# Performance work log

Measured on AMD Instinct MI355X. Metric: run time of the kernel, lower is better.

## Reference

```python
import jax, jax.numpy as jnp
import numpy as np

B, S, D = 2, 2048, 2048
N_HEADS = 16
HEAD_DIM = D // N_HEADS  # 128


def apply_rotary(xq, xk, cos, sin):
    # xq, xk: [B, S, H, HD]; cos, sin: [S, HD//2]
    def rot(t):
        tr = t.reshape(t.shape[:-1] + (HEAD_DIM // 2, 2))
        r, i = tr[..., 0], tr[..., 1]
        c = cos[None, :, None, :]  # [1, S, 1, HD//2]
        s = sin[None, :, None, :]
        out_r = r * c - i * s
        out_i = r * s + i * c
        return jnp.stack([out_r, out_i], axis=-1).reshape(t.shape)
    return rot(xq), rot(xk)


def setup_inputs() -> dict:
    key = jax.random.key(0)
    k1, k2, k3 = jax.random.split(key, 3)
    x = jax.random.normal(k1, (B, S, D), dtype=jnp.float32)
    wqkv = jax.random.normal(k2, (3 * D, D), dtype=jnp.float32) * (D ** -0.5)
    wo = jax.random.normal(k3, (D, D), dtype=jnp.float32) * (D ** -0.5)
    # rotary tables, standard llama theta=10000
    inv_freq = 1.0 / (10000.0 ** (jnp.arange(0, HEAD_DIM, 2, dtype=jnp.float32) / HEAD_DIM))
    t = jnp.arange(S, dtype=jnp.float32)
    freqs = jnp.outer(t, inv_freq)  # [S, HD//2]
    freqs_cos = jnp.cos(freqs)
    freqs_sin = jnp.sin(freqs)
    # causal additive mask [1, 1, S, S]
    causal = jnp.tril(jnp.ones((S, S), dtype=bool))
    mask = jnp.where(causal, 0.0, -jnp.inf).astype(jnp.float32)[None, None]
    return {"x": x, "freqs_cos": freqs_cos, "freqs_sin": freqs_sin,
            "mask": mask, "wqkv": wqkv, "wo": wo, "input_pos": 0}


def reference(x, freqs_cos, freqs_sin, mask, wqkv, wo, input_pos):
    # fused QKV projection (Linear: x @ W^T)
    qkv = jnp.einsum('bsd,ed->bse', x, wqkv)  # [B, S, 3D]
    xq, xk, xv = jnp.split(qkv, 3, axis=-1)
    xq = xq.reshape(B, S, N_HEADS, HEAD_DIM)
    xk = xk.reshape(B, S, N_HEADS, HEAD_DIM)
    xv = xv.reshape(B, S, N_HEADS, HEAD_DIM)
    xq, xk = apply_rotary(xq, xk, freqs_cos, freqs_sin)
    # SDPA (kv_cache is None; input_pos unused)
    scale = HEAD_DIM ** -0.5
    scores = jnp.einsum('bqhd,bkhd->bhqk', xq, xk) * scale + mask
    attn = jax.nn.softmax(scores, axis=-1)
    out = jnp.einsum('bhqk,bkhd->bqhd', attn, xv).reshape(B, S, D)
    return jnp.einsum('bsd,ed->bse', out, wo)
```

## Files before the change

kernel.cpp:

```cpp
#include <hip/hip_runtime.h>

#define B_ 2
#define S_ 2048
#define D_ 2048
#define H_ 16
#define DH_ 128
#define E3_ (3*D_)

typedef __attribute__((ext_vector_type(4))) float f32x4;
typedef __attribute__((ext_vector_type(8))) short bf16x8;

__device__ __forceinline__ unsigned short f2bf(float f) {
  unsigned u = __float_as_uint(f);
  u += 0x7fff + ((u >> 16) & 1);
  return (unsigned short)(u >> 16);
}
__device__ __forceinline__ float bf2f(unsigned short h) {
  return __uint_as_float(((unsigned)h) << 16);
}
__device__ __forceinline__ unsigned cvt_pk_bf16(float lo, float hi) {
  unsigned r;
  asm("v_cvt_pk_bf16_f32 %0, %1, %2" : "=v"(r) : "v"(lo), "v"(hi));
  return r;
}

__global__ void cast_f32_bf16(const float* __restrict__ in, unsigned short* __restrict__ out, int n4) {
  int i = blockIdx.x * 256 + threadIdx.x;
  if (i >= n4) return;
  float4 v = reinterpret_cast<const float4*>(in)[i];
  ushort4 o;
  o.x = f2bf(v.x); o.y = f2bf(v.y); o.z = f2bf(v.z); o.w = f2bf(v.w);
  reinterpret_cast<ushort4*>(out)[i] = o;
}

template<typename OutT>
__global__ __launch_bounds__(256) void gemm_bt(const unsigned short* __restrict__ A,
                                               const unsigned short* __restrict__ Bm,
                                               OutT* __restrict__ C,
                                               unsigned short* __restrict__ Vt,
                                               int Mdim, int Ndim, int Kdim) {
  __shared__ __align__(16) unsigned short As[128*64];
  __shared__ __align__(16) unsigned short Bs[128*64];
  const int t = threadIdx.x;
  const int lane = t & 63;
  const int w = t >> 6;
  const int wm = w >> 1, wn = w & 1;
  const int l16 = lane & 15, lg = lane >> 4;
  const int bm = blockIdx.y, bn = blockIdx.x;

  f32x4 acc[4][4] = {};
  const int e0 = t * 8;

  for (int k0 = 0; k0 < Kdim; k0 += 64) {
#pragma unroll
    for (int it = 0; it < 4; ++it) {
      int e = e0 + it * 2048;
      int row = e >> 6;
      int g = (e >> 3) & 7;
      int gs = g ^ (row & 7);
      const unsigned short* ga = A  + (size_t)(bm*128 + row) * Kdim + k0 + gs*8;
      const unsigned short* gb = Bm + (size_t)(bn*128 + row) * Kdim + k0 + gs*8;
      __builtin_amdgcn_global_load_lds((const __attribute__((address_space(1))) unsigned int*)ga,
                                       (__attribute__((address_space(3))) unsigned int*)(&As[e]), 16, 0, 0);
      __builtin_amdgcn_global_load_lds((const __attribute__((address_space(1))) unsigned int*)gb,
                                       (__attribute__((address_space(3))) unsigned int*)(&Bs[e]), 16, 0, 0);
    }
    __syncthreads();
#pragma unroll
    for (int kk = 0; kk < 2; ++kk) {
      bf16x8 a[4], b[4];
#pragma unroll
      for (int mi = 0; mi < 4; ++mi) {
        int row = wm*64 + mi*16 + l16;
        int gw = kk*4 + lg;
        a[mi] = *reinterpret_cast<const bf16x8*>(&As[row*64 + ((gw ^ (row & 7))<<3)]);
      }
#pragma unroll
      for (int ni = 0; ni < 4; ++ni) {
        int row = wn*64 + ni*16 + l16;
        int gw = kk*4 + lg;
        b[ni] = *reinterpret_cast<const bf16x8*>(&Bs[row*64 + ((gw ^ (row & 7))<<3)]);
      }
#pragma unroll
      for (int mi = 0; mi < 4; ++mi)
#pragma unroll
        for (int ni = 0; ni < 4; ++ni)
          acc[mi][ni] = __builtin_amdgcn_mfma_f32_16x16x32_bf16(a[mi], b[ni], acc[mi][ni], 0, 0, 0);
    }
    __syncthreads();
  }
  if constexpr (sizeof(OutT) == 2) {
    if (Vt != nullptr && bn >= 32) {
#pragma unroll
      for (int mi = 0; mi < 4; ++mi) {
#pragma unroll
        for (int ni = 0; ni < 4; ++ni) {
          int colv = bn*128 + wn*64 + ni*16 + l16 - 2*D_;
          int h = colv >> 7, d = colv & 127;
          int row0 = bm*128 + wm*64 + mi*16 + lg*4;
          int b = row0 >> 11, s = row0 & 2047;
          ushort4 v4;
          v4.x = f2bf(acc[mi][ni][0]);
          v4.y = f2bf(acc[mi][ni][1]);
          v4.z = f2bf(acc[mi][ni][2]);
          v4.w = f2bf(acc[mi][ni][3]);
          *reinterpret_cast<ushort4*>(&Vt[(((size_t)(b*H_ + h))*DH_ + d)*S_ + s]) = v4;
        }
      }
      return;
    }
  }
#pragma unroll
  for (int mi = 0; mi < 4; ++mi) {
#pragma unroll
    for (int ni = 0; ni < 4; ++ni) {
      int col = bn*128 + wn*64 + ni*16 + l16;
      int row0 = bm*128 + wm*64 + mi*16 + lg*4;
#pragma unroll
      for (int r = 0; r < 4; ++r) {
        float v = acc[mi][ni][r];
        size_t idx = (size_t)(row0 + r) * Ndim + col;
        if constexpr (sizeof(OutT) == 2) C[idx] = f2bf(v);
        else C[idx] = v;
      }
    }
  }
}

__global__ void rope_qk(const unsigned short* __restrict__ qkv,
                        const float* __restrict__ cosT, const float* __restrict__ sinT,
                        unsigned short* __restrict__ Q, unsigned short* __restrict__ K) {
  const float SCL = 0.08838834764831845f * 1.4426950408889634f;
  int d = threadIdx.x;
  int h = blockIdx.x;
  int s = blockIdx.y;
  int b = blockIdx.z;
  size_t rowb = ((size_t)(b*S_ + s)) * E3_;
  int j = d >> 1;
  float c  = cosT[s*64 + j];
  float sn = sinT[s*64 + j];
  int de = d & ~1, odd = d & 1;
  float x0 = bf2f(qkv[rowb + h*DH_ + de]);
  float x1 = bf2f(qkv[rowb + h*DH_ + de + 1]);
  float oq = odd ? (x0*sn + x1*c) : (x0*c - x1*sn);
  size_t qo = (((size_t)(b*H_ + h)) * S_ + s) * DH_ + d;
  Q[qo] = f2bf(oq * SCL);
  float y0 = bf2f(qkv[rowb + D_ + h*DH_ + de]);
  float y1 = bf2f(qkv[rowb + D_ + h*DH_ + de + 1]);
  float ok = odd ? (y0*sn + y1*c) : (y0*c - y1*sn);
  K[qo] = f2bf(ok);
}

#define NQT 32
__global__ __launch_bounds__(512) void attn(const unsigned short* __restrict__ Q,
                                            const unsigned short* __restrict__ K,
                                            const unsigned short* __restrict__ Vt,
                                            unsigned short* __restrict__ O) {
  __shared__ __align__(16) unsigned short Ks[64*128];
  __shared__ __align__(16) unsigned short Vs[128*64];
  __shared__ __align__(16) unsigned short Plds[8][16*64];
  const int x = blockIdx.x;
  const int bh = blockIdx.y;
  const int b = bh >> 4, h = bh & 15;
  const int t = threadIdx.x;
  const int lane = t & 63;
  const int w = t >> 6;
  const int wg = w >> 2;
  const int wi = w & 3;
  const int l16 = lane & 15, lg = lane >> 4;
  const int qt = wg ? (NQT - 1 - x) : x;
  const int q0 = qt * 64 + wi * 16;
  const unsigned short* Qh = Q  + (size_t)bh * S_ * DH_;
  const unsigned short* Kh = K  + (size_t)bh * S_ * DH_;
  const unsigned short* Vh = Vt + (size_t)bh * DH_ * S_;

  bf16x8 aq[4];
#pragma unroll
  for (int kk = 0; kk < 4; ++kk)
    aq[kk] = *reinterpret_cast<const bf16x8*>(Qh + (size_t)(q0 + l16)*DH_ + kk*32 + lg*8);

  f32x4 o[8] = {};
  float mrun = -1e30f, lrun = 0.f;
  const int ntiles = NQT - x;

  for (int tile = 0; tile < ntiles; ++tile) {
    const int kv0 = tile * 64;
#pragma unroll
    for (int it = 0; it < 2; ++it) {
      int e = t*8 + it*4096;
      int row = e >> 7;
      int gslot = (e >> 3) & 15;
      int gsrc = gslot ^ (row & 7);
      const unsigned short* ga = Kh + (size_t)(kv0 + row) * DH_ + gsrc*8;
      __builtin_amdgcn_global_load_lds((const __attribute__((address_space(1))) unsigned int*)ga,
                                       (__attribute__((address_space(3))) unsigned int*)(&Ks[e]), 16, 0, 0);
    }
#pragma unroll
    for (int it = 0; it < 2; ++it) {
      int e = t*8 + it*4096;
      int d = e >> 6;
      int gslot = (e >> 3) & 7;
      int gsrc = gslot ^ (d & 7);
      const unsigned short* gv = Vh + (size_t)d * S_ + kv0 + gsrc*8;
      __builtin_amdgcn_global_load_lds((const __attribute__((address_space(1))) unsigned int*)gv,
                                       (__attribute__((address_space(3))) unsigned int*)(&Vs[e]), 16, 0, 0);
    }
    __syncthreads();

    if (tile <= qt) {
      f32x4 sc[4] = {};
#pragma unroll
      for (int kk = 0; kk < 4; ++kk) {
#pragma unroll
        for (int n = 0; n < 4; ++n) {
          int row = n*16 + l16;
          int g = kk*4 + lg;
          bf16x8 bk = *reinterpret_cast<const bf16x8*>(&Ks[row*128 + ((g ^ (row & 7))<<3)]);
          sc[n] = __builtin_amdgcn_mfma_f32_16x16x32_bf16(bk, aq[kk], sc[n], 0, 0, 0);
        }
      }
      if (tile == qt) {
        int qrow = q0 + l16;
#pragma unroll
        for (int n = 0; n < 4; ++n)
#pragma unroll
          for (int r = 0; r < 4; ++r) {
            int kidx = kv0 + n*16 + lg*4 + r;
            sc[n][r] = (kidx > qrow) ? -1e30f : sc[n][r];
          }
      }
      float mt = sc[0][0];
#pragma unroll
      for (int n = 0; n < 4; ++n)
#pragma unroll
        for (int r = 0; r < 4; ++r) mt = fmaxf(mt, sc[n][r]);
      mt = fmaxf(mt, __shfl_xor(mt, 16));
      mt = fmaxf(mt, __shfl_xor(mt, 32));
      if (__any(mt > mrun + 8.f)) {
        float mnew = fmaxf(mrun, mt);
        float alpha = __builtin_amdgcn_exp2f(mrun - mnew);
        mrun = mnew;
        lrun *= alpha;
        float ar[4];
#pragma unroll
        for (int r = 0; r < 4; ++r) ar[r] = __shfl(alpha, lg*4 + r);
#pragma unroll
        for (int n2 = 0; n2 < 8; ++n2)
#pragma unroll
          for (int r = 0; r < 4; ++r) o[n2][r] *= ar[r];
      }
      float rs = 0.f;
      unsigned pk[4][2];
#pragma unroll
      for (int n = 0; n < 4; ++n) {
        float p0 = __builtin_amdgcn_exp2f(sc[n][0] - mrun);
        float p1 = __builtin_amdgcn_exp2f(sc[n][1] - mrun);
        float p2 = __builtin_amdgcn_exp2f(sc[n][2] - mrun);
        float p3 = __builtin_amdgcn_exp2f(sc[n][3] - mrun);
        rs += (p0 + p1) + (p2 + p3);
        pk[n][0] = cvt_pk_bf16(p0, p1);
        pk[n][1] = cvt_pk_bf16(p2, p3);
      }
      rs += __shfl_xor(rs, 16);
      rs += __shfl_xor(rs, 32);
      lrun += rs;
      unsigned short* Pw = &Plds[w][0];
      char* Pb = (char*)Pw + l16*128;
#pragma unroll
      for (int n = 0; n < 4; ++n) {
        int sslot = (n*4 + lg) ^ (l16 & 14);
        *reinterpret_cast<uint2*>(Pb + sslot*8) = make_uint2(pk[n][0], pk[n][1]);
      }
      bf16x8 pa[2];
#pragma unroll
      for (int kk2 = 0; kk2 < 2; ++kk2) {
        int tp = (kk2*4 + lg) ^ ((l16 >> 1) & 7);
        pa[kk2] = *reinterpret_cast<const bf16x8*>(Pb + tp*16);
      }
#pragma unroll
      for (int kk2 = 0; kk2 < 2; ++kk2) {
#pragma unroll
        for (int n2 = 0; n2 < 8; ++n2) {
          int d = n2*16 + l16;
          int g = kk2*4 + lg;
          bf16x8 bv = *reinterpret_cast<const bf16x8*>(&Vs[d*64 + ((g ^ (d & 7))<<3)]);
          o[n2] = __builtin_amdgcn_mfma_f32_16x16x32_bf16(pa[kk2], bv, o[n2], 0, 0, 0);
        }
      }
    }
    __syncthreads();
  }
  float linv = 1.f / lrun;
  float lr[4];
#pragma unroll
  for (int r = 0; r < 4; ++r) lr[r] = __shfl(linv, lg*4 + r);
  size_t ob = ((size_t)b * S_) * D_;
#pragma unroll
  for (int n2 = 0; n2 < 8; ++n2) {
#pragma unroll
    for (int r = 0; r < 4; ++r) {
      int rowq = q0 + lg*4 + r;
      int d = n2*16 + l16;
      O[ob + (size_t)rowq * D_ + h*DH_ + d] = f2bf(o[n2][r] * lr[r]);
    }
  }
}

extern "C" void kernel_launch(void* const* d_in, const int* in_sizes, int n_in,
                              void* d_out, int out_size, void* d_ws, size_t ws_size,
                              hipStream_t stream) {
  const float* x    = (const float*)d_in[0];
  const float* fcos = (const float*)d_in[1];
  const float* fsin = (const float*)d_in[2];
  const float* wqkv = (const float*)d_in[4];
  const float* wo   = (const float*)d_in[5];
  float* out = (float*)d_out;
  char* ws = (char*)d_ws;

  unsigned short* xb    = (unsigned short*)(ws);
  unsigned short* wqkvb = (unsigned short*)(ws + 16777216);
  unsigned short* wob   = (unsigned short*)(ws + 41943040);
  unsigned short* qkv   = (unsigned short*)(ws + 50331648);
  unsigned short* Qb    = (unsigned short*)(ws + 100663296);
  unsigned short* Kb    = (unsigned short*)(ws + 117440512);
  unsigned short* Vtb   = (unsigned short*)(ws + 134217728);
  unsigned short* attn_out = xb;

  cast_f32_bf16<<<dim3(2097152/256), 256, 0, stream>>>(x, xb, 2097152);
  cast_f32_bf16<<<dim3(3145728/256), 256, 0, stream>>>(wqkv, wqkvb, 3145728);
  cast_f32_bf16<<<dim3(1048576/256), 256, 0, stream>>>(wo, wob, 1048576);

  gemm_bt<unsigned short><<<dim3(6144/128, 4096/128), 256, 0, stream>>>(xb, wqkvb, qkv, Vtb, 4096, 6144, 2048);
  rope_qk<<<dim3(16, 2048, 2), 128, 0, stream>>>(qkv, fcos, fsin, Qb, Kb);
  attn<<<dim3(16, 32), 512, 0, stream>>>(Qb, Kb, Vtb, attn_out);
  gemm_bt<float><<<dim3(2048/128, 4096/128), 256, 0, stream>>>(attn_out, wob, out, (unsigned short*)nullptr, 4096, 2048, 2048);
}
```

Measured before the change: 271.2 us.

## Fuse RoPE into QKV GEMM epilogue and double-buffer attention KV tiles

RoPE and the Q scaling move into the QKV GEMM epilogue, using a lane shuffle to fetch the paired element, so Q and K are written directly in head-major layout. This removes the separate rope kernel and the round trip through the intermediate qkv buffer. The attention kernel now double-buffers its K/V LDS tiles so the next tile's loads overlap compute, with one barrier per iteration. It also remaps block indices across XCDs and raises wave priority around the MFMA sections. The cost is more shared memory per block and per-element cos/sin loads in the GEMM epilogue.

```diff
diff --git a/kernel.cpp b/kernel.cpp
--- a/kernel.cpp
+++ b/kernel.cpp
@@ -33,12 +33,14 @@
   reinterpret_cast<ushort4*>(out)[i] = o;
 }
 
-template<typename OutT>
-__global__ __launch_bounds__(256) void gemm_bt(const unsigned short* __restrict__ A,
-                                               const unsigned short* __restrict__ Bm,
-                                               OutT* __restrict__ C,
-                                               unsigned short* __restrict__ Vt,
-                                               int Mdim, int Ndim, int Kdim) {
+__global__ __launch_bounds__(256) void gemm_qkv(const unsigned short* __restrict__ A,
+                                                const unsigned short* __restrict__ Bm,
+                                                unsigned short* __restrict__ Qb,
+                                                unsigned short* __restrict__ Kb,
+                                                unsigned short* __restrict__ Vt,
+                                                const float* __restrict__ cosT,
+                                                const float* __restrict__ sinT) {
+  const int Kdim = 2048;
   __shared__ __align__(16) unsigned short As[128*64];
   __shared__ __align__(16) unsigned short Bs[128*64];
   const int t = threadIdx.x;
@@ -89,26 +91,107 @@
     }
     __syncthreads();
   }
-  if constexpr (sizeof(OutT) == 2) {
-    if (Vt != nullptr && bn >= 32) {
+
+  if (bn >= 32) {
+#pragma unroll
+    for (int mi = 0; mi < 4; ++mi) {
+#pragma unroll
+      for (int ni = 0; ni < 4; ++ni) {
+        int colv = (bn - 32)*128 + wn*64 + ni*16 + l16;
+        int h = colv >> 7, d = colv & 127;
+        int row0 = bm*128 + wm*64 + mi*16 + lg*4;
+        int b = row0 >> 11, s = row0 & 2047;
+        ushort4 v4;
+        v4.x = f2bf(acc[mi][ni][0]);
+        v4.y = f2bf(acc[mi][ni][1]);
+        v4.z = f2bf(acc[mi][ni][2]);
+        v4.w = f2bf(acc[mi][ni][3]);
+        *reinterpret_cast<ushort4*>(&Vt[(((size_t)(b*H_ + h))*DH_ + d)*S_ + s]) = v4;
+      }
+    }
+  } else {
+    const float SCLQ = 0.08838834764831845f * 1.4426950408889634f;
+    const bool isQ = (bn < 16);
+    unsigned short* dst = isQ ? Qb : Kb;
+    const float sgn = (l16 & 1) ? 1.f : -1.f;
+#pragma unroll
+    for (int ni = 0; ni < 4; ++ni) {
+      int colh = (bn & 15)*128 + wn*64 + ni*16 + l16;
+      int h = colh >> 7, d = colh & 127;
+      int j = d >> 1;
 #pragma unroll
       for (int mi = 0; mi < 4; ++mi) {
-#pragma unroll
-        for (int ni = 0; ni < 4; ++ni) {
-          int colv = bn*128 + wn*64 + ni*16 + l16 - 2*D_;
-          int h = colv >> 7, d = colv & 127;
-          int row0 = bm*128 + wm*64 + mi*16 + lg*4;
-          int b = row0 >> 11, s = row0 & 2047;
-          ushort4 v4;
-          v4.x = f2bf(acc[mi][ni][0]);
-          v4.y = f2bf(acc[mi][ni][1]);
-          v4.z = f2bf(acc[mi][ni][2]);
-          v4.w = f2bf(acc[mi][ni][3]);
-          *reinterpret_cast<ushort4*>(&Vt[(((size_t)(b*H_ + h))*DH_ + d)*S_ + s]) = v4;
+        int row0 = bm*128 + wm*64 + mi*16 + lg*4;
+#pragma unroll
+        for (int r = 0; r < 4; ++r) {
+          int row = row0 + r;
+          int b = row >> 11, s = row & 2047;
+          float c  = cosT[s*64 + j];
+          float sn = sinT[s*64 + j];
+          float v = acc[mi][ni][r];
+          float p = __shfl_xor(v, 1);
+          float ov = fmaf(v, c, p * sn * sgn);
+          if (isQ) ov *= SCLQ;
+          dst[(((size_t)(b*H_ + h))*S_ + s)*DH_ + d] = f2bf(ov);
         }
       }
-      return;
-    }
+    }
+  }
+}
+
+__global__ __launch_bounds__(256) void gemm_bt(const unsigned short* __restrict__ A,
+                                               const unsigned short* __restrict__ Bm,
+                                               float* __restrict__ C,
+                                               int Ndim, int Kdim) {
+  __shared__ __align__(16) unsigned short As[128*64];
+  __shared__ __align__(16) unsigned short Bs[128*64];
+  const int t = threadIdx.x;
+  const int lane = t & 63;
+  const int w = t >> 6;
+  const int wm = w >> 1, wn = w & 1;
+  const int l16 = lane & 15, lg = lane >> 4;
+  const int bm = blockIdx.y, bn = blockIdx.x;
+
+  f32x4 acc[4][4] = {};
+  const int e0 = t * 8;
+
+  for (int k0 = 0; k0 < Kdim; k0 += 64) {
+#pragma unroll
+    for (int it = 0; it < 4; ++it) {
+      int e = e0 + it * 2048;
+      int row = e >> 6;
+      int g = (e >> 3) & 7;
+      int gs = g ^ (row & 7);
+      const unsigned short* ga = A  + (size_t)(bm*128 + row) * Kdim + k0 + gs*8;
+      const unsigned short* gb = Bm + (size_t)(bn*128 + row) * Kdim + k0 + gs*8;
+      __builtin_amdgcn_global_load_lds((const __attribute__((address_space(1))) unsigned int*)ga,
+                                       (__attribute__((address_space(3))) unsigned int*)(&As[e]), 16, 0, 0);
+      __builtin_amdgcn_global_load_lds((const __attribute__((address_space(1))) unsigned int*)gb,
+                                       (__attribute__((address_space(3))) unsigned int*)(&Bs[e]), 16, 0, 0);
+    }
+    __syncthreads();
+#pragma unroll
+    for (int kk = 0; kk < 2; ++kk) {
+      bf16x8 a[4], b[4];
+#pragma unroll
+      for (int mi = 0; mi < 4; ++mi) {
+        int row = wm*64 + mi*16 + l16;
+        int gw = kk*4 + lg;
+        a[mi] = *reinterpret_cast<const bf16x8*>(&As[row*64 + ((gw ^ (row & 7))<<3)]);
+      }
+#pragma unroll
+      for (int ni = 0; ni < 4; ++ni) {
+        int row = wn*64 + ni*16 + l16;
+        int gw = kk*4 + lg;
+        b[ni] = *reinterpret_cast<const bf16x8*>(&Bs[row*64 + ((gw ^ (row & 7))<<3)]);
+      }
+#pragma unroll
+      for (int mi = 0; mi < 4; ++mi)
+#pragma unroll
+        for (int ni = 0; ni < 4; ++ni)
+          acc[mi][ni] = __builtin_amdgcn_mfma_f32_16x16x32_bf16(a[mi], b[ni], acc[mi][ni], 0, 0, 0);
+    }
+    __syncthreads();
   }
 #pragma unroll
   for (int mi = 0; mi < 4; ++mi) {
@@ -117,38 +200,10 @@
       int col = bn*128 + wn*64 + ni*16 + l16;
       int row0 = bm*128 + wm*64 + mi*16 + lg*4;
 #pragma unroll
-      for (int r = 0; r < 4; ++r) {
-        float v = acc[mi][ni][r];
-        size_t idx = (size_t)(row0 + r) * Ndim + col;
-        if constexpr (sizeof(OutT) == 2) C[idx] = f2bf(v);
-        else C[idx] = v;
-      }
-    }
-  }
-}
-
-__global__ void rope_qk(const unsigned short* __restrict__ qkv,
-                        const float* __restrict__ cosT, const float* __restrict__ sinT,
-                        unsigned short* __restrict__ Q, unsigned short* __restrict__ K) {
-  const float SCL = 0.08838834764831845f * 1.4426950408889634f;
-  int d = threadIdx.x;
-  int h = blockIdx.x;
-  int s = blockIdx.y;
-  int b = blockIdx.z;
-  size_t rowb = ((size_t)(b*S_ + s)) * E3_;
-  int j = d >> 1;
-  float c  = cosT[s*64 + j];
-  float sn = sinT[s*64 + j];
-  int de = d & ~1, odd = d & 1;
-  float x0 = bf2f(qkv[rowb + h*DH_ + de]);
-  float x1 = bf2f(qkv[rowb + h*DH_ + de + 1]);
-  float oq = odd ? (x0*sn + x1*c) : (x0*c - x1*sn);
-  size_t qo = (((size_t)(b*H_ + h)) * S_ + s) * DH_ + d;
-  Q[qo] = f2bf(oq * SCL);
-  float y0 = bf2f(qkv[rowb + D_ + h*DH_ + de]);
-  float y1 = bf2f(qkv[rowb + D_ + h*DH_ + de + 1]);
-  float ok = odd ? (y0*sn + y1*c) : (y0*c - y1*sn);
-  K[qo] = f2bf(ok);
+      for (int r = 0; r < 4; ++r)
+        C[(size_t)(row0 + r) * Ndim + col] = acc[mi][ni][r];
+    }
+  }
 }
 
 #define NQT 32
@@ -156,19 +211,21 @@
                                             const unsigned short* __restrict__ K,
                                             const unsigned short* __restrict__ Vt,
                                             unsigned short* __restrict__ O) {
-  __shared__ __align__(16) unsigned short Ks[64*128];
-  __shared__ __align__(16) unsigned short Vs[128*64];
+  __shared__ __align__(16) unsigned short Ks[2][64*128];
+  __shared__ __align__(16) unsigned short Vs[2][128*64];
   __shared__ __align__(16) unsigned short Plds[8][16*64];
-  const int x = blockIdx.x;
-  const int bh = blockIdx.y;
+  const int orig = blockIdx.y * gridDim.x + blockIdx.x;
+  const int wg = (orig & 7) * 64 + (orig >> 3);
+  const int x = wg & 15;
+  const int bh = wg >> 4;
   const int b = bh >> 4, h = bh & 15;
   const int t = threadIdx.x;
   const int lane = t & 63;
   const int w = t >> 6;
-  const int wg = w >> 2;
+  const int wg8 = w >> 2;
   const int wi = w & 3;
   const int l16 = lane & 15, lg = lane >> 4;
-  const int qt = wg ? (NQT - 1 - x) : x;
+  const int qt = wg8 ? (NQT - 1 - x) : x;
   const int q0 = qt * 64 + wi * 16;
   const unsigned short* Qh = Q  + (size_t)bh * S_ * DH_;
   const unsigned short* Kh = K  + (size_t)bh * S_ * DH_;
@@ -183,42 +240,55 @@
   float mrun = -1e30f, lrun = 0.f;
   const int ntiles = NQT - x;
 
+#define STAGE_KV(TILE)                                                                              \
+  {                                                                                                 \
+    const int kv0s = (TILE) * 64;                                                                   \
+    unsigned short* Kd = &Ks[(TILE) & 1][0];                                                        \
+    unsigned short* Vd = &Vs[(TILE) & 1][0];                                                        \
+    _Pragma("unroll")                                                                               \
+    for (int it = 0; it < 2; ++it) {                                                                \
+      int e = t*8 + it*4096;                                                                        \
+      int row = e >> 7;                                                                             \
+      int gslot = (e >> 3) & 15;                                                                    \
+      int gsrc = gslot ^ (row & 7);                                                                 \
+      const unsigned short* ga = Kh + (size_t)(kv0s + row) * DH_ + gsrc*8;                          \
+      __builtin_amdgcn_global_load_lds((const __attribute__((address_space(1))) unsigned int*)ga,   \
+                                       (__attribute__((address_space(3))) unsigned int*)(&Kd[e]), 16, 0, 0); \
+    }                                                                                               \
+    _Pragma("unroll")                                                                               \
+    for (int it = 0; it < 2; ++it) {                                                                \
+      int e = t*8 + it*4096;                                                                        \
+      int dd = e >> 6;                                                                              \
+      int gslot = (e >> 3) & 7;                                                                     \
+      int gsrc = gslot ^ (dd & 7);                                                                  \
+      const unsigned short* gv = Vh + (size_t)dd * S_ + kv0s + gsrc*8;                              \
+      __builtin_amdgcn_global_load_lds((const __attribute__((address_space(1))) unsigned int*)gv,   \
+                                       (__attribute__((address_space(3))) unsigned int*)(&Vd[e]), 16, 0, 0); \
+    }                                                                                               \
+  }
+
+  STAGE_KV(0);
+
   for (int tile = 0; tile < ntiles; ++tile) {
+    __syncthreads();
+    if (tile + 1 < ntiles) STAGE_KV(tile + 1);
     const int kv0 = tile * 64;
-#pragma unroll
-    for (int it = 0; it < 2; ++it) {
-      int e = t*8 + it*4096;
-      int row = e >> 7;
-      int gslot = (e >> 3) & 15;
-      int gsrc = gslot ^ (row & 7);
-      const unsigned short* ga = Kh + (size_t)(kv0 + row) * DH_ + gsrc*8;
-      __builtin_amdgcn_global_load_lds((const __attribute__((address_space(1))) unsigned int*)ga,
-                                       (__attribute__((address_space(3))) unsigned int*)(&Ks[e]), 16, 0, 0);
-    }
-#pragma unroll
-    for (int it = 0; it < 2; ++it) {
-      int e = t*8 + it*4096;
-      int d = e >> 6;
-      int gslot = (e >> 3) & 7;
-      int gsrc = gslot ^ (d & 7);
-      const unsigned short* gv = Vh + (size_t)d * S_ + kv0 + gsrc*8;
-      __builtin_amdgcn_global_load_lds((const __attribute__((address_space(1))) unsigned int*)gv,
-                                       (__attribute__((address_space(3))) unsigned int*)(&Vs[e]), 16, 0, 0);
-    }
-    __syncthreads();
+    const int buf = tile & 1;
 
     if (tile <= qt) {
       f32x4 sc[4] = {};
+      __builtin_amdgcn_s_setprio(1);
 #pragma unroll
       for (int kk = 0; kk < 4; ++kk) {
 #pragma unroll
         for (int n = 0; n < 4; ++n) {
           int row = n*16 + l16;
           int g = kk*4 + lg;
-          bf16x8 bk = *reinterpret_cast<const bf16x8*>(&Ks[row*128 + ((g ^ (row & 7))<<3)]);
+          bf16x8 bk = *reinterpret_cast<const bf16x8*>(&Ks[buf][row*128 + ((g ^ (row & 7))<<3)]);
           sc[n] = __builtin_amdgcn_mfma_f32_16x16x32_bf16(bk, aq[kk], sc[n], 0, 0, 0);
         }
       }
+      __builtin_amdgcn_s_setprio(0);
       if (tile == qt) {
         int qrow = q0 + l16;
 #pragma unroll
@@ -277,18 +347,19 @@
         int tp = (kk2*4 + lg) ^ ((l16 >> 1) & 7);
         pa[kk2] = *reinterpret_cast<const bf16x8*>(Pb + tp*16);
       }
+      __builtin_amdgcn_s_setprio(1);
 #pragma unroll
       for (int kk2 = 0; kk2 < 2; ++kk2) {
 #pragma unroll
         for (int n2 = 0; n2 < 8; ++n2) {
           int d = n2*16 + l16;
           int g = kk2*4 + lg;
-          bf16x8 bv = *reinterpret_cast<const bf16x8*>(&Vs[d*64 + ((g ^ (d & 7))<<3)]);
+          bf16x8 bv = *reinterpret_cast<const bf16x8*>(&Vs[buf][d*64 + ((g ^ (d & 7))<<3)]);
           o[n2] = __builtin_amdgcn_mfma_f32_16x16x32_bf16(pa[kk2], bv, o[n2], 0, 0, 0);
         }
       }
-    }
-    __syncthreads();
+      __builtin_amdgcn_s_setprio(0);
+    }
   }
   float linv = 1.f / lrun;
   float lr[4];
@@ -320,18 +391,16 @@
   unsigned short* xb    = (unsigned short*)(ws);
   unsigned short* wqkvb = (unsigned short*)(ws + 16777216);
   unsigned short* wob   = (unsigned short*)(ws + 41943040);
-  unsigned short* qkv   = (unsigned short*)(ws + 50331648);
-  unsigned short* Qb    = (unsigned short*)(ws + 100663296);
-  unsigned short* Kb    = (unsigned short*)(ws + 117440512);
-  unsigned short* Vtb   = (unsigned short*)(ws + 134217728);
+  unsigned short* Qb    = (unsigned short*)(ws + 50331648);
+  unsigned short* Kb    = (unsigned short*)(ws + 67108864);
+  unsigned short* Vtb   = (unsigned short*)(ws + 83886080);
   unsigned short* attn_out = xb;
 
   cast_f32_bf16<<<dim3(2097152/256), 256, 0, stream>>>(x, xb, 2097152);
   cast_f32_bf16<<<dim3(3145728/256), 256, 0, stream>>>(wqkv, wqkvb, 3145728);
   cast_f32_bf16<<<dim3(1048576/256), 256, 0, stream>>>(wo, wob, 1048576);
 
-  gemm_bt<unsigned short><<<dim3(6144/128, 4096/128), 256, 0, stream>>>(xb, wqkvb, qkv, Vtb, 4096, 6144, 2048);
-  rope_qk<<<dim3(16, 2048, 2), 128, 0, stream>>>(qkv, fcos, fsin, Qb, Kb);
+  gemm_qkv<<<dim3(48, 32), 256, 0, stream>>>(xb, wqkvb, Qb, Kb, Vtb, fcos, fsin);
   attn<<<dim3(16, 32), 512, 0, stream>>>(Qb, Kb, Vtb, attn_out);
-  gemm_bt<float><<<dim3(2048/128, 4096/128), 256, 0, stream>>>(attn_out, wob, out, (unsigned short*)nullptr, 4096, 2048, 2048);
-}
+  gemm_bt<<<dim3(16, 32), 256, 0, stream>>>(attn_out, wob, out, 2048, 2048);
+}
```

Result: slower. 360.5 us (+32.9%).
